# Kernel optimization log

Measured on AMD Instinct MI355X. Metric: run time of the kernel, lower is better.

The kernel has to match this reference:

```python
import jax, jax.numpy as jnp
import numpy as np
import math

B, N, IN_DIM, EMBED, HEADS = 1, 96, 128, 128, 4
HD = EMBED // HEADS  # head_dim = 32


def _layernorm(x, g, b, eps=1e-5):
    mu = jnp.mean(x, axis=-1, keepdims=True)
    var = jnp.var(x, axis=-1, keepdims=True)
    return (x - mu) * jax.lax.rsqrt(var + eps) * g + b


def setup_inputs() -> dict:
    key = jax.random.key(0)
    ks = jax.random.split(key, 3)
    x = jax.random.normal(ks[0], (B, N, N, IN_DIM), dtype=jnp.float32)
    W = jax.random.normal(ks[1], (IN_DIM, EMBED), dtype=jnp.float32) / math.sqrt(IN_DIM)
    b = jnp.zeros((EMBED,), jnp.float32)
    ln_g = jnp.ones((HD,), jnp.float32)
    ln_b = jnp.zeros((HD,), jnp.float32)
    Wf = jax.random.normal(ks[2], (IN_DIM + EMBED, EMBED), dtype=jnp.float32) / math.sqrt(IN_DIM + EMBED)
    bf = jnp.zeros((EMBED,), jnp.float32)
    ln2_g = jnp.ones((EMBED,), jnp.float32)
    ln2_b = jnp.zeros((EMBED,), jnp.float32)
    return {"x": x, "W": W, "b": b, "ln_g": ln_g, "ln_b": ln_b,
            "Wf": Wf, "bf": bf, "ln2_g": ln2_g, "ln2_b": ln2_b}


def reference(x, W, b, ln_g, ln_b, Wf, bf, ln2_g, ln2_b):
    # NOTE: original torch module shares ONE Linear across q/k/v1/v2 and ONE
    # LayerNorm across norms[0..2] (ModuleList([m]*k) aliases the module).
    Bq, Nq = x.shape[0], x.shape[1]
    p = (jnp.einsum('bxyi,ie->bxye', x, W) + b).reshape(Bq, Nq, Nq, HEADS, HD)
    pn = _layernorm(p, ln_g, ln_b)                         # q == k (shared params)
    scores = jnp.einsum('bxahd,bayhd->bxayh', pn, pn) / math.sqrt(HD)
    att = jax.nn.softmax(scores, axis=2)                   # softmax over a
    x_upd = jnp.einsum('bxahd,bayhd->bxayhd', p, p)        # v1 == v2 == p
    x_upd = _layernorm(x_upd, ln_g, ln_b)                  # shared norm params
    agg = jnp.einsum('bxayh,bxayhd->bxyhd', att, x_upd).reshape(Bq, Nq, Nq, EMBED)
    cat = jnp.concatenate([x, agg], axis=-1)
    out = jnp.einsum('bxyc,ce->bxye', cat, Wf) + bf
    return _layernorm(out, ln2_g, ln2_b)
```

## Files before the change

kernel.cpp:

```cpp
#include <hip/hip_runtime.h>
#include <math.h>

#define NTOK 96
#define EMBED 128
#define HEADS 4
#define HD 32
#define NROW (NTOK*NTOK)
#define YT 16
#define NYT (NTOK/YT)

__global__ __launch_bounds__(128) void k_proj(
    const float* __restrict__ x, const float* __restrict__ W,
    const float* __restrict__ b,
    float* __restrict__ pT, float* __restrict__ murT) {
  const int r0 = blockIdx.x * 4;
  const int X  = r0 / NTOK;
  const int y0 = r0 % NTOK;
  const int e  = threadIdx.x;
  __shared__ float xt[EMBED][4];
  #pragma unroll
  for (int k = 0; k < 4; ++k)
    xt[e][k] = x[(size_t)(r0 + k) * EMBED + e];
  __syncthreads();

  const float bias = b[e];
  float a0 = bias, a1 = bias, a2 = bias, a3 = bias;
  #pragma unroll 8
  for (int i = 0; i < EMBED; ++i) {
    const float wv = W[(size_t)i * EMBED + e];
    const float4 c = *(const float4*)&xt[i][0];
    a0 = fmaf(wv, c.x, a0); a1 = fmaf(wv, c.y, a1);
    a2 = fmaf(wv, c.z, a2); a3 = fmaf(wv, c.w, a3);
  }

  const int h = e >> 5;
  float accs[4] = {a0, a1, a2, a3};
  #pragma unroll
  for (int k = 0; k < 4; ++k) {
    pT[((size_t)(y0 + k) * NTOK + X) * EMBED + e] = accs[k];
    float s1 = accs[k], s2 = accs[k] * accs[k];
    #pragma unroll
    for (int m_ = 1; m_ < 32; m_ <<= 1) {
      s1 += __shfl_xor(s1, m_, 64);
      s2 += __shfl_xor(s2, m_, 64);
    }
    if ((e & 31) == 0) {
      const float mu = s1 * (1.f / HD);
      const float var = fmaxf(s2 * (1.f / HD) - mu * mu, 0.f);
      float2 v; v.x = mu; v.y = rsqrtf(var + 1e-5f);
      *(float2*)&murT[(((size_t)(y0 + k) * NTOK + X) * HEADS + h) * 2] = v;
    }
  }
}

__device__ __forceinline__ void sc_elem(float e, float f, float g, float b,
    float rE, float pE, float rF, float pF,
    float& s, float& m, float& q, float& t) {
  const float uE = fmaf(e, rE, -pE);
  const float en = fmaf(uE, g, b);
  const float uF = fmaf(f, rF, -pF);
  const float fn = fmaf(uF, g, b);
  s = fmaf(en, fn, s);
  t = e * f;
  m += t;
  q = fmaf(t, t, q);
}

#define SC_QUAD(E4, F4, G4, B4, T4) \
  sc_elem(E4.x, F4.x, G4.x, B4.x, rE, pE, rF, pF, s, m, q, T4.x); \
  sc_elem(E4.y, F4.y, G4.y, B4.y, rE, pE, rF, pF, s, m, q, T4.y); \
  sc_elem(E4.z, F4.z, G4.z, B4.z, rE, pE, rF, pF, s, m, q, T4.z); \
  sc_elem(E4.w, F4.w, G4.w, B4.w, rE, pE, rF, pF, s, m, q, T4.w);

#define AGG_QUAD(A4, T4) \
  A4.x = fmaf(w, T4.x, A4.x); A4.y = fmaf(w, T4.y, A4.y); \
  A4.z = fmaf(w, T4.z, A4.z); A4.w = fmaf(w, T4.w, A4.w);

#define SCALE_QUAD(A4) \
  A4.x *= scale; A4.y *= scale; A4.z *= scale; A4.w *= scale;

#define RED_QUAD(A4, MASK) \
  A4.x += __shfl_xor(A4.x, MASK, 64); A4.y += __shfl_xor(A4.y, MASK, 64); \
  A4.z += __shfl_xor(A4.z, MASK, 64); A4.w += __shfl_xor(A4.w, MASK, 64);

__global__ __launch_bounds__(256) void k_fused(
    const float* __restrict__ pT, const float* __restrict__ murT,
    const float* __restrict__ ln_g, const float* __restrict__ ln_b,
    const float* __restrict__ x, const float* __restrict__ Wf,
    const float* __restrict__ bf, const float* __restrict__ g2,
    const float* __restrict__ b2, float* __restrict__ out) {
  const int bid = blockIdx.x;
  const int X   = bid / NYT;
  const int y0  = (bid % NYT) * YT;

  const int tid = threadIdx.x;
  const int y   = tid >> 4;
  const int t16 = tid & 15;
  const int ds  = t16 >> 3;
  const int da  = t16 & 7;
  const int yy  = y0 + y;
  const int eoff = ds * 16;

  __shared__ float e_sm[NTOK][36];
  __shared__ float mur_sm[NTOK][2];
  __shared__ float xt_sm[EMBED][20];
  __shared__ float agg_t[EMBED][20];
  __shared__ float g_sm[HD], b_sm[HD];
  __shared__ float red_sm[4][8][2];

  #pragma unroll
  for (int i = 0; i < 8; ++i) {
    const int g = tid + i * 256;
    const int yl = g >> 7, c = g & 127;
    xt_sm[c][yl] = x[((size_t)(X * NTOK + y0 + yl)) * EMBED + c];
  }
  if (tid < HD) { g_sm[tid] = ln_g[tid]; b_sm[tid] = ln_b[tid]; }

  for (int H = 0; H < HEADS; ++H) {
    __syncthreads();
    #pragma unroll
    for (int i = 0; i < 3; ++i) {
      const int g = tid + i * 256;
      const int a = g >> 3, qq = g & 7;
      *(float4*)&e_sm[a][qq * 4] =
          *(const float4*)&pT[((size_t)a * NTOK + X) * EMBED + H * HD + qq * 4];
    }
    if (tid < NTOK) {
      const float2 v = *(const float2*)&murT[(((size_t)tid * NTOK + X) * HEADS + H) * 2];
      mur_sm[tid][0] = v.x; mur_sm[tid][1] = v.y;
    }
    __syncthreads();

    const float4 g0 = *(const float4*)&g_sm[eoff];
    const float4 g1 = *(const float4*)&g_sm[eoff + 4];
    const float4 g2v = *(const float4*)&g_sm[eoff + 8];
    const float4 g3 = *(const float4*)&g_sm[eoff + 12];
    const float4 b0 = *(const float4*)&b_sm[eoff];
    const float4 b1 = *(const float4*)&b_sm[eoff + 4];
    const float4 b2v = *(const float4*)&b_sm[eoff + 8];
    const float4 b3 = *(const float4*)&b_sm[eoff + 12];

    const float* fbase = pT + (size_t)yy * NTOK * EMBED + H * HD + eoff;
    const float* mbase = murT + ((size_t)yy * NTOK * HEADS + H) * 2;

    float4 acc0 = {0,0,0,0}, acc1 = {0,0,0,0}, acc2 = {0,0,0,0}, acc3 = {0,0,0,0};
    float den = 0.f, c = 0.f, mx = -1e30f;

    #pragma unroll 2
    for (int ia = 0; ia < 12; ++ia) {
      const int a = ia * 8 + da;
      const float4* fp = (const float4*)(fbase + (size_t)a * EMBED);
      const float4 f0 = fp[0], f1 = fp[1], f2 = fp[2], f3 = fp[3];
      const float2 mrF = *(const float2*)(mbase + (size_t)a * (HEADS * 2));
      const float muE = mur_sm[a][0], rE = mur_sm[a][1];
      const float rF = mrF.y;
      const float pE = muE * rE;
      const float pF = mrF.x * rF;
      const float4 e0 = *(const float4*)&e_sm[a][eoff];
      const float4 e1 = *(const float4*)&e_sm[a][eoff + 4];
      const float4 e2 = *(const float4*)&e_sm[a][eoff + 8];
      const float4 e3 = *(const float4*)&e_sm[a][eoff + 12];

      float s = 0.f, m = 0.f, q = 0.f;
      float4 t0, t1, t2, t3;
      SC_QUAD(e0, f0, g0, b0, t0);
      SC_QUAD(e1, f1, g1, b1, t1);
      SC_QUAD(e2, f2, g2v, b2v, t2);
      SC_QUAD(e3, f3, g3, b3, t3);

      s += __shfl_xor(s, 8, 64);
      m += __shfl_xor(m, 8, 64);
      q += __shfl_xor(q, 8, 64);

      const float mu = m * (1.f / HD);
      const float var = fmaxf(fmaf(-mu, mu, q * (1.f / HD)), 0.f);
      const float r = rsqrtf(var + 1e-5f);
      const float sc = s * 0.17677669529663687f;

      float mc = sc;
      mc = fmaxf(mc, __shfl_xor(mc, 1, 64));
      mc = fmaxf(mc, __shfl_xor(mc, 2, 64));
      mc = fmaxf(mc, __shfl_xor(mc, 4, 64));
      const float nmx = fmaxf(mx, mc);
      const float scale = __expf(mx - nmx);
      mx = nmx;
      const float ex = __expf(sc - mx);
      const float w = ex * r;
      den = fmaf(den, scale, ex);
      c   = fmaf(c,   scale, w * mu);
      SCALE_QUAD(acc0); SCALE_QUAD(acc1); SCALE_QUAD(acc2); SCALE_QUAD(acc3);
      AGG_QUAD(acc0, t0);
      AGG_QUAD(acc1, t1);
      AGG_QUAD(acc2, t2);
      AGG_QUAD(acc3, t3);
    }

    #pragma unroll
    for (int mask = 1; mask <= 4; mask <<= 1) {
      den += __shfl_xor(den, mask, 64);
      c   += __shfl_xor(c,   mask, 64);
      RED_QUAD(acc0, mask);
      RED_QUAD(acc1, mask);
      RED_QUAD(acc2, mask);
      RED_QUAD(acc3, mask);
    }

    if (da == 0) {
      const float inv = 1.f / den;
      float ov[16];
      ov[0]  = fmaf(g0.x, (acc0.x - c) * inv, b0.x);
      ov[1]  = fmaf(g0.y, (acc0.y - c) * inv, b0.y);
      ov[2]  = fmaf(g0.z, (acc0.z - c) * inv, b0.z);
      ov[3]  = fmaf(g0.w, (acc0.w - c) * inv, b0.w);
      ov[4]  = fmaf(g1.x, (acc1.x - c) * inv, b1.x);
      ov[5]  = fmaf(g1.y, (acc1.y - c) * inv, b1.y);
      ov[6]  = fmaf(g1.z, (acc1.z - c) * inv, b1.z);
      ov[7]  = fmaf(g1.w, (acc1.w - c) * inv, b1.w);
      ov[8]  = fmaf(g2v.x, (acc2.x - c) * inv, b2v.x);
      ov[9]  = fmaf(g2v.y, (acc2.y - c) * inv, b2v.y);
      ov[10] = fmaf(g2v.z, (acc2.z - c) * inv, b2v.z);
      ov[11] = fmaf(g2v.w, (acc2.w - c) * inv, b2v.w);
      ov[12] = fmaf(g3.x, (acc3.x - c) * inv, b3.x);
      ov[13] = fmaf(g3.y, (acc3.y - c) * inv, b3.y);
      ov[14] = fmaf(g3.z, (acc3.z - c) * inv, b3.z);
      ov[15] = fmaf(g3.w, (acc3.w - c) * inv, b3.w);
      #pragma unroll
      for (int j = 0; j < 16; ++j)
        agg_t[H * HD + eoff + j][y] = ov[j];
    }
  }
  __syncthreads();

  const int e  = tid & 127;
  const int rh = tid >> 7;
  const float bias = bf[e];
  float acc8[8];
  #pragma unroll
  for (int k = 0; k < 8; ++k) acc8[k] = bias;

  #pragma unroll 4
  for (int i = 0; i < EMBED; ++i) {
    const float wv = Wf[(size_t)i * EMBED + e];
    const float4 c0 = *(const float4*)&xt_sm[i][rh * 8];
    const float4 c1 = *(const float4*)&xt_sm[i][rh * 8 + 4];
    acc8[0] = fmaf(wv, c0.x, acc8[0]); acc8[1] = fmaf(wv, c0.y, acc8[1]);
    acc8[2] = fmaf(wv, c0.z, acc8[2]); acc8[3] = fmaf(wv, c0.w, acc8[3]);
    acc8[4] = fmaf(wv, c1.x, acc8[4]); acc8[5] = fmaf(wv, c1.y, acc8[5]);
    acc8[6] = fmaf(wv, c1.z, acc8[6]); acc8[7] = fmaf(wv, c1.w, acc8[7]);
  }
  #pragma unroll 4
  for (int i = 0; i < EMBED; ++i) {
    const float wv = Wf[(size_t)(EMBED + i) * EMBED + e];
    const float4 c0 = *(const float4*)&agg_t[i][rh * 8];
    const float4 c1 = *(const float4*)&agg_t[i][rh * 8 + 4];
    acc8[0] = fmaf(wv, c0.x, acc8[0]); acc8[1] = fmaf(wv, c0.y, acc8[1]);
    acc8[2] = fmaf(wv, c0.z, acc8[2]); acc8[3] = fmaf(wv, c0.w, acc8[3]);
    acc8[4] = fmaf(wv, c1.x, acc8[4]); acc8[5] = fmaf(wv, c1.y, acc8[5]);
    acc8[6] = fmaf(wv, c1.z, acc8[6]); acc8[7] = fmaf(wv, c1.w, acc8[7]);
  }

  const int wid = tid >> 6;
  #pragma unroll
  for (int k = 0; k < 8; ++k) {
    float s1 = acc8[k], s2 = acc8[k] * acc8[k];
    #pragma unroll
    for (int m_ = 1; m_ < 64; m_ <<= 1) {
      s1 += __shfl_xor(s1, m_, 64);
      s2 += __shfl_xor(s2, m_, 64);
    }
    if ((tid & 63) == 0) { red_sm[wid][k][0] = s1; red_sm[wid][k][1] = s2; }
  }
  __syncthreads();

  const float gg = g2[e], bb = b2[e];
  #pragma unroll
  for (int k = 0; k < 8; ++k) {
    const float S1 = red_sm[wid][k][0] + red_sm[wid ^ 1][k][0];
    const float S2 = red_sm[wid][k][1] + red_sm[wid ^ 1][k][1];
    const float mu = S1 * (1.f / EMBED);
    const float var = fmaxf(S2 * (1.f / EMBED) - mu * mu, 0.f);
    const float rstd = rsqrtf(var + 1e-5f);
    out[((size_t)(X * NTOK + y0 + rh * 8 + k)) * EMBED + e] =
        (acc8[k] - mu) * rstd * gg + bb;
  }
}

extern "C" void kernel_launch(void* const* d_in, const int* in_sizes, int n_in,
                              void* d_out, int out_size, void* d_ws, size_t ws_size,
                              hipStream_t stream) {
  const float* x    = (const float*)d_in[0];
  const float* W    = (const float*)d_in[1];
  const float* b    = (const float*)d_in[2];
  const float* ln_g = (const float*)d_in[3];
  const float* ln_b = (const float*)d_in[4];
  const float* Wf   = (const float*)d_in[5];
  const float* bf   = (const float*)d_in[6];
  const float* g2   = (const float*)d_in[7];
  const float* b2   = (const float*)d_in[8];
  float* out = (float*)d_out;

  float* pT   = (float*)d_ws;
  float* murT = pT + (size_t)NROW * EMBED;

  k_proj<<<NROW / 4, 128, 0, stream>>>(x, W, b, pT, murT);
  k_fused<<<NTOK * NYT, 256, 0, stream>>>(pT, murT, ln_g, ln_b,
                                          x, Wf, bf, g2, b2, out);
}
```

Measured before the change: 112.6 us.

## Process two heads concurrently with 512-thread blocks and reorder block-to-X mapping

```diff
diff --git a/kernel.cpp b/kernel.cpp
--- a/kernel.cpp
+++ b/kernel.cpp
@@ -83,54 +83,60 @@
   A4.x += __shfl_xor(A4.x, MASK, 64); A4.y += __shfl_xor(A4.y, MASK, 64); \
   A4.z += __shfl_xor(A4.z, MASK, 64); A4.w += __shfl_xor(A4.w, MASK, 64);
 
-__global__ __launch_bounds__(256) void k_fused(
+__global__ __launch_bounds__(512) void k_fused(
     const float* __restrict__ pT, const float* __restrict__ murT,
     const float* __restrict__ ln_g, const float* __restrict__ ln_b,
     const float* __restrict__ x, const float* __restrict__ Wf,
     const float* __restrict__ bf, const float* __restrict__ g2,
     const float* __restrict__ b2, float* __restrict__ out) {
   const int bid = blockIdx.x;
-  const int X   = bid / NYT;
-  const int y0  = (bid % NYT) * YT;
+  const int X   = bid % NTOK;
+  const int y0  = (bid / NTOK) * YT;
 
   const int tid = threadIdx.x;
-  const int y   = tid >> 4;
-  const int t16 = tid & 15;
-  const int ds  = t16 >> 3;
-  const int da  = t16 & 7;
+  const int hh  = tid >> 8;
+  const int y   = (tid >> 4) & 15;
+  const int ds  = (tid >> 3) & 1;
+  const int da  = tid & 7;
   const int yy  = y0 + y;
   const int eoff = ds * 16;
 
-  __shared__ float e_sm[NTOK][36];
-  __shared__ float mur_sm[NTOK][2];
+  __shared__ float e_sm[2][NTOK][36];
+  __shared__ float mur_sm[2][NTOK][2];
   __shared__ float xt_sm[EMBED][20];
   __shared__ float agg_t[EMBED][20];
   __shared__ float g_sm[HD], b_sm[HD];
-  __shared__ float red_sm[4][8][2];
-
-  #pragma unroll
-  for (int i = 0; i < 8; ++i) {
-    const int g = tid + i * 256;
-    const int yl = g >> 7, c = g & 127;
-    xt_sm[c][yl] = x[((size_t)(X * NTOK + y0 + yl)) * EMBED + c];
+  __shared__ float red_sm[8][4][2];
+
+  #pragma unroll
+  for (int i = 0; i < 4; ++i) {
+    const int g = tid + i * 512;
+    const int yl = g >> 7, col = g & 127;
+    xt_sm[col][yl] = x[((size_t)(X * NTOK + y0 + yl)) * EMBED + col];
   }
   if (tid < HD) { g_sm[tid] = ln_g[tid]; b_sm[tid] = ln_b[tid]; }
 
-  for (int H = 0; H < HEADS; ++H) {
+  for (int hl = 0; hl < 2; ++hl) {
     __syncthreads();
     #pragma unroll
     for (int i = 0; i < 3; ++i) {
-      const int g = tid + i * 256;
-      const int a = g >> 3, qq = g & 7;
-      *(float4*)&e_sm[a][qq * 4] =
-          *(const float4*)&pT[((size_t)a * NTOK + X) * EMBED + H * HD + qq * 4];
-    }
-    if (tid < NTOK) {
-      const float2 v = *(const float2*)&murT[(((size_t)tid * NTOK + X) * HEADS + H) * 2];
-      mur_sm[tid][0] = v.x; mur_sm[tid][1] = v.y;
+      const int g = tid + i * 512;
+      const int h2 = g >> 9? (g >= 768 ? 1 : 1) : (g >= 768 ? 1 : 0);
+      const int hd2 = (g >= 768) ? 1 : 0;
+      const int rem = g - hd2 * 768;
+      const int a = rem >> 3, qq = rem & 7;
+      (void)h2;
+      *(float4*)&e_sm[hd2][a][qq * 4] =
+          *(const float4*)&pT[((size_t)a * NTOK + X) * EMBED + (hl * 2 + hd2) * HD + qq * 4];
+    }
+    if (tid < 192) {
+      const int a = tid >> 1, h2s = tid & 1;
+      *(float2*)&mur_sm[h2s][a][0] =
+          *(const float2*)&murT[(((size_t)a * NTOK + X) * HEADS + hl * 2 + h2s) * 2];
     }
     __syncthreads();
 
+    const int H = hl * 2 + hh;
     const float4 g0 = *(const float4*)&g_sm[eoff];
     const float4 g1 = *(const float4*)&g_sm[eoff + 4];
     const float4 g2v = *(const float4*)&g_sm[eoff + 8];
@@ -144,7 +150,7 @@
     const float* mbase = murT + ((size_t)yy * NTOK * HEADS + H) * 2;
 
     float4 acc0 = {0,0,0,0}, acc1 = {0,0,0,0}, acc2 = {0,0,0,0}, acc3 = {0,0,0,0};
-    float den = 0.f, c = 0.f, mx = -1e30f;
+    float den = 0.f, cc = 0.f, mx = -1e30f;
 
     #pragma unroll 2
     for (int ia = 0; ia < 12; ++ia) {
@@ -152,14 +158,14 @@
       const float4* fp = (const float4*)(fbase + (size_t)a * EMBED);
       const float4 f0 = fp[0], f1 = fp[1], f2 = fp[2], f3 = fp[3];
       const float2 mrF = *(const float2*)(mbase + (size_t)a * (HEADS * 2));
-      const float muE = mur_sm[a][0], rE = mur_sm[a][1];
+      const float muE = mur_sm[hh][a][0], rE = mur_sm[hh][a][1];
       const float rF = mrF.y;
       const float pE = muE * rE;
       const float pF = mrF.x * rF;
-      const float4 e0 = *(const float4*)&e_sm[a][eoff];
-      const float4 e1 = *(const float4*)&e_sm[a][eoff + 4];
-      const float4 e2 = *(const float4*)&e_sm[a][eoff + 8];
-      const float4 e3 = *(const float4*)&e_sm[a][eoff + 12];
+      const float4 e0 = *(const float4*)&e_sm[hh][a][eoff];
+      const float4 e1 = *(const float4*)&e_sm[hh][a][eoff + 4];
+      const float4 e2 = *(const float4*)&e_sm[hh][a][eoff + 8];
+      const float4 e3 = *(const float4*)&e_sm[hh][a][eoff + 12];
 
       float s = 0.f, m = 0.f, q = 0.f;
       float4 t0, t1, t2, t3;
@@ -187,7 +193,7 @@
       const float ex = __expf(sc - mx);
       const float w = ex * r;
       den = fmaf(den, scale, ex);
-      c   = fmaf(c,   scale, w * mu);
+      cc  = fmaf(cc,  scale, w * mu);
       SCALE_QUAD(acc0); SCALE_QUAD(acc1); SCALE_QUAD(acc2); SCALE_QUAD(acc3);
       AGG_QUAD(acc0, t0);
       AGG_QUAD(acc1, t1);
@@ -198,7 +204,7 @@
     #pragma unroll
     for (int mask = 1; mask <= 4; mask <<= 1) {
       den += __shfl_xor(den, mask, 64);
-      c   += __shfl_xor(c,   mask, 64);
+      cc  += __shfl_xor(cc,  mask, 64);
       RED_QUAD(acc0, mask);
       RED_QUAD(acc1, mask);
       RED_QUAD(acc2, mask);
@@ -208,22 +214,22 @@
     if (da == 0) {
       const float inv = 1.f / den;
       float ov[16];
-      ov[0]  = fmaf(g0.x, (acc0.x - c) * inv, b0.x);
-      ov[1]  = fmaf(g0.y, (acc0.y - c) * inv, b0.y);
-      ov[2]  = fmaf(g0.z, (acc0.z - c) * inv, b0.z);
-      ov[3]  = fmaf(g0.w, (acc0.w - c) * inv, b0.w);
-      ov[4]  = fmaf(g1.x, (acc1.x - c) * inv, b1.x);
-      ov[5]  = fmaf(g1.y, (acc1.y - c) * inv, b1.y);
-      ov[6]  = fmaf(g1.z, (acc1.z - c) * inv, b1.z);
-      ov[7]  = fmaf(g1.w, (acc1.w - c) * inv, b1.w);
-      ov[8]  = fmaf(g2v.x, (acc2.x - c) * inv, b2v.x);
-      ov[9]  = fmaf(g2v.y, (acc2.y - c) * inv, b2v.y);
-      ov[10] = fmaf(g2v.z, (acc2.z - c) * inv, b2v.z);
-      ov[11] = fmaf(g2v.w, (acc2.w - c) * inv, b2v.w);
-      ov[12] = fmaf(g3.x, (acc3.x - c) * inv, b3.x);
-      ov[13] = fmaf(g3.y, (acc3.y - c) * inv, b3.y);
-      ov[14] = fmaf(g3.z, (acc3.z - c) * inv, b3.z);
-      ov[15] = fmaf(g3.w, (acc3.w - c) * inv, b3.w);
+      ov[0]  = fmaf(g0.x, (acc0.x - cc) * inv, b0.x);
+      ov[1]  = fmaf(g0.y, (acc0.y - cc) * inv, b0.y);
+      ov[2]  = fmaf(g0.z, (acc0.z - cc) * inv, b0.z);
+      ov[3]  = fmaf(g0.w, (acc0.w - cc) * inv, b0.w);
+      ov[4]  = fmaf(g1.x, (acc1.x - cc) * inv, b1.x);
+      ov[5]  = fmaf(g1.y, (acc1.y - cc) * inv, b1.y);
+      ov[6]  = fmaf(g1.z, (acc1.z - cc) * inv, b1.z);
+      ov[7]  = fmaf(g1.w, (acc1.w - cc) * inv, b1.w);
+      ov[8]  = fmaf(g2v.x, (acc2.x - cc) * inv, b2v.x);
+      ov[9]  = fmaf(g2v.y, (acc2.y - cc) * inv, b2v.y);
+      ov[10] = fmaf(g2v.z, (acc2.z - cc) * inv, b2v.z);
+      ov[11] = fmaf(g2v.w, (acc2.w - cc) * inv, b2v.w);
+      ov[12] = fmaf(g3.x, (acc3.x - cc) * inv, b3.x);
+      ov[13] = fmaf(g3.y, (acc3.y - cc) * inv, b3.y);
+      ov[14] = fmaf(g3.z, (acc3.z - cc) * inv, b3.z);
+      ov[15] = fmaf(g3.w, (acc3.w - cc) * inv, b3.w);
       #pragma unroll
       for (int j = 0; j < 16; ++j)
         agg_t[H * HD + eoff + j][y] = ov[j];
@@ -234,35 +240,27 @@
   const int e  = tid & 127;
   const int rh = tid >> 7;
   const float bias = bf[e];
-  float acc8[8];
-  #pragma unroll
-  for (int k = 0; k < 8; ++k) acc8[k] = bias;
-
-  #pragma unroll 4
+  float acc4[4] = {bias, bias, bias, bias};
+
+  #pragma unroll 8
   for (int i = 0; i < EMBED; ++i) {
     const float wv = Wf[(size_t)i * EMBED + e];
-    const float4 c0 = *(const float4*)&xt_sm[i][rh * 8];
-    const float4 c1 = *(const float4*)&xt_sm[i][rh * 8 + 4];
-    acc8[0] = fmaf(wv, c0.x, acc8[0]); acc8[1] = fmaf(wv, c0.y, acc8[1]);
-    acc8[2] = fmaf(wv, c0.z, acc8[2]); acc8[3] = fmaf(wv, c0.w, acc8[3]);
-    acc8[4] = fmaf(wv, c1.x, acc8[4]); acc8[5] = fmaf(wv, c1.y, acc8[5]);
-    acc8[6] = fmaf(wv, c1.z, acc8[6]); acc8[7] = fmaf(wv, c1.w, acc8[7]);
-  }
-  #pragma unroll 4
+    const float4 c0 = *(const float4*)&xt_sm[i][rh * 4];
+    acc4[0] = fmaf(wv, c0.x, acc4[0]); acc4[1] = fmaf(wv, c0.y, acc4[1]);
+    acc4[2] = fmaf(wv, c0.z, acc4[2]); acc4[3] = fmaf(wv, c0.w, acc4[3]);
+  }
+  #pragma unroll 8
   for (int i = 0; i < EMBED; ++i) {
     const float wv = Wf[(size_t)(EMBED + i) * EMBED + e];
-    const float4 c0 = *(const float4*)&agg_t[i][rh * 8];
-    const float4 c1 = *(const float4*)&agg_t[i][rh * 8 + 4];
-    acc8[0] = fmaf(wv, c0.x, acc8[0]); acc8[1] = fmaf(wv, c0.y, acc8[1]);
-    acc8[2] = fmaf(wv, c0.z, acc8[2]); acc8[3] = fmaf(wv, c0.w, acc8[3]);
-    acc8[4] = fmaf(wv, c1.x, acc8[4]); acc8[5] = fmaf(wv, c1.y, acc8[5]);
-    acc8[6] = fmaf(wv, c1.z, acc8[6]); acc8[7] = fmaf(wv, c1.w, acc8[7]);
+    const float4 c0 = *(const float4*)&agg_t[i][rh * 4];
+    acc4[0] = fmaf(wv, c0.x, acc4[0]); acc4[1] = fmaf(wv, c0.y, acc4[1]);
+    acc4[2] = fmaf(wv, c0.z, acc4[2]); acc4[3] = fmaf(wv, c0.w, acc4[3]);
   }
 
   const int wid = tid >> 6;
   #pragma unroll
-  for (int k = 0; k < 8; ++k) {
-    float s1 = acc8[k], s2 = acc8[k] * acc8[k];
+  for (int k = 0; k < 4; ++k) {
+    float s1 = acc4[k], s2 = acc4[k] * acc4[k];
     #pragma unroll
     for (int m_ = 1; m_ < 64; m_ <<= 1) {
       s1 += __shfl_xor(s1, m_, 64);
@@ -274,14 +272,14 @@
 
   const float gg = g2[e], bb = b2[e];
   #pragma unroll
-  for (int k = 0; k < 8; ++k) {
+  for (int k = 0; k < 4; ++k) {
     const float S1 = red_sm[wid][k][0] + red_sm[wid ^ 1][k][0];
     const float S2 = red_sm[wid][k][1] + red_sm[wid ^ 1][k][1];
     const float mu = S1 * (1.f / EMBED);
     const float var = fmaxf(S2 * (1.f / EMBED) - mu * mu, 0.f);
     const float rstd = rsqrtf(var + 1e-5f);
-    out[((size_t)(X * NTOK + y0 + rh * 8 + k)) * EMBED + e] =
-        (acc8[k] - mu) * rstd * gg + bb;
+    out[((size_t)(X * NTOK + y0 + rh * 4 + k)) * EMBED + e] =
+        (acc4[k] - mu) * rstd * gg + bb;
   }
 }
 
@@ -303,6 +301,6 @@
   float* murT = pT + (size_t)NROW * EMBED;
 
   k_proj<<<NROW / 4, 128, 0, stream>>>(x, W, b, pT, murT);
-  k_fused<<<NTOK * NYT, 256, 0, stream>>>(pT, murT, ln_g, ln_b,
+  k_fused<<<NTOK * NYT, 512, 0, stream>>>(pT, murT, ln_g, ln_b,
                                           x, Wf, bf, g2, b2, out);
 }
```

New measurement: 129.1 us. +14.6%, slower.
